# Kernel optimization log

Hardware: AMD Instinct MI355X
Metric: run time of the kernel (lower is better)

The kernel has to match this reference:

```python
import jax, jax.numpy as jnp
import numpy as np

N_NODES = 50000
N_EDGES = 800000
IN_DIM = 512
HID_DIM = 128


def setup_inputs() -> dict:
    key = jax.random.key(0)
    k1, k2, k3 = jax.random.split(key, 3)
    x = jax.random.normal(k1, (N_NODES, IN_DIM), dtype=jnp.float32)
    edge_index = jax.random.randint(k2, (2, N_EDGES), 0, N_NODES, dtype=jnp.int32)
    # GCNConv weight (glorot-ish scale) and bias
    W = jax.random.normal(k3, (IN_DIM, HID_DIM), dtype=jnp.float32) * (1.0 / np.sqrt(IN_DIM))
    b = jnp.zeros((HID_DIM,), dtype=jnp.float32)
    # PReLU per-channel slope, torch default init 0.25
    prelu_w = jnp.full((HID_DIM,), 0.25, dtype=jnp.float32)
    return {"x": x, "edge_index": edge_index, "W": W, "b": b, "prelu_w": prelu_w}


def reference(x, edge_index, W, b, prelu_w):
    N = x.shape[0]
    # 1) linear transform first (GCNConv transforms then aggregates)
    h = x @ W  # [N, H]
    # 2) add self-loops
    loop = jnp.arange(N, dtype=edge_index.dtype)
    src = jnp.concatenate([edge_index[0], loop])  # [E+N]
    dst = jnp.concatenate([edge_index[1], loop])  # [E+N]
    # 3) symmetric degree normalization deg^-1/2 (self-loops guarantee deg>=1)
    deg = jax.ops.segment_sum(jnp.ones_like(dst, dtype=h.dtype), dst, num_segments=N)
    dinv = jax.lax.rsqrt(deg)
    norm = dinv[src] * dinv[dst]  # [E+N]
    # 4) gather-scale-scatter aggregation
    msg = h[src] * norm[:, None]  # [E+N, H]
    out = jax.ops.segment_sum(msg, dst, num_segments=N) + b  # [N, H]
    # 5) per-channel PReLU
    return jnp.where(out > 0, out, prelu_w * out)
```

## Files before the change

kernel.cpp:

```cpp
#include <hip/hip_runtime.h>

#define IN_DIM 512
#define HID 128
#define BK 64

#define RANGE 98
#define NB_ 511
#define NBLK 200
#define SEGCAP 2048

typedef float f4 __attribute__((ext_vector_type(4)));
typedef short bf8 __attribute__((ext_vector_type(8)));

__device__ inline unsigned short f2bf(float f) {
    unsigned u = __float_as_uint(f);
    unsigned r = (u + 0x7FFFu + ((u >> 16) & 1u)) >> 16;
    return (unsigned short)r;
}
__device__ inline float bf2f(unsigned short u) {
    return __uint_as_float(((unsigned)u) << 16);
}
__device__ inline int xcd_perm(int blk) {
    return (blk & 7) * (NBLK / 8) + (blk >> 3);
}

__global__ __launch_bounds__(256) void k_count(const int* __restrict__ dst,
                                               int* __restrict__ cmat, int E) {
    __shared__ int bins[NB_];
    const int blk = blockIdx.x, t = threadIdx.x;
    const int chunk = (((E + NBLK - 1) / NBLK) + 3) & ~3;
    const int start = blk * chunk;
    const int end = min(E, start + chunk);
    for (int i = t; i < NB_; i += 256) bins[i] = 0;
    __syncthreads();
    if (start < E) {
        int nvec = (end - start) >> 2;
        for (int i = t; i < nvec; i += 256) {
            int4 d4 = *(const int4*)(dst + start + i * 4);
            atomicAdd(&bins[d4.x / RANGE], 1);
            atomicAdd(&bins[d4.y / RANGE], 1);
            atomicAdd(&bins[d4.z / RANGE], 1);
            atomicAdd(&bins[d4.w / RANGE], 1);
        }
        for (int i = start + nvec * 4 + t; i < end; i += 256)
            atomicAdd(&bins[dst[i] / RANGE], 1);
    }
    __syncthreads();
    const int p = xcd_perm(blk);
    for (int j = t; j < NB_; j += 256) cmat[j * NBLK + p] = bins[j];
}

__global__ __launch_bounds__(256) void k_cscan(int* __restrict__ cmat,
                                               int* __restrict__ tot) {
    __shared__ int s[256];
    const int j = blockIdx.x, t = threadIdx.x;
    int v = (t < NBLK) ? cmat[j * NBLK + t] : 0;
    s[t] = v;
    __syncthreads();
    for (int off = 1; off < 256; off <<= 1) {
        int y = (t >= off) ? s[t - off] : 0;
        __syncthreads();
        s[t] += y;
        __syncthreads();
    }
    if (t < NBLK) cmat[j * NBLK + t] = s[t] - v;
    if (t == 255) tot[j] = s[255];
}

__global__ __launch_bounds__(512) void k_tscan(const int* __restrict__ tot,
                                               int* __restrict__ bbase,
                                               int* __restrict__ rowStart,
                                               int N, int E) {
    __shared__ int s[512];
    int t = threadIdx.x;
    int v = (t < NB_) ? tot[t] : 0;
    s[t] = v;
    __syncthreads();
    for (int off = 1; off < 512; off <<= 1) {
        int y = (t >= off) ? s[t - off] : 0;
        __syncthreads();
        s[t] += y;
        __syncthreads();
    }
    if (t < NB_) bbase[t] = s[t] - v;
    if (t == 0) rowStart[N] = E;
}

__global__ __launch_bounds__(256) void k_scatter(const int* __restrict__ src,
                                                 const int* __restrict__ dst,
                                                 const int* __restrict__ cmat,
                                                 const int* __restrict__ bbase,
                                                 unsigned* __restrict__ ebuf, int E) {
    __shared__ int cur[NB_];
    const int blk = blockIdx.x, t = threadIdx.x;
    const int p = xcd_perm(blk);
    for (int j = t; j < NB_; j += 256) cur[j] = bbase[j] + cmat[j * NBLK + p];
    __syncthreads();
    const int chunk = (((E + NBLK - 1) / NBLK) + 3) & ~3;
    const int start = blk * chunk;
    const int end = min(E, start + chunk);
    if (start >= E) return;
    int nvec = (end - start) >> 2;
    for (int i = t; i < nvec; i += 256) {
        int4 s4 = *(const int4*)(src + start + i * 4);
        int4 d4 = *(const int4*)(dst + start + i * 4);
        int ss[4] = {s4.x, s4.y, s4.z, s4.w};
        int dd[4] = {d4.x, d4.y, d4.z, d4.w};
#pragma unroll
        for (int k = 0; k < 4; k++) {
            int b = dd[k] / RANGE;
            int ld = dd[k] - b * RANGE;
            int pos = atomicAdd(&cur[b], 1);
            ebuf[pos] = ((unsigned)ld << 25) | (unsigned)ss[k];
        }
    }
    for (int i = start + nvec * 4 + t; i < end; i += 256) {
        int d = dst[i];
        int b = d / RANGE;
        int ld = d - b * RANGE;
        int pos = atomicAdd(&cur[b], 1);
        ebuf[pos] = ((unsigned)ld << 25) | (unsigned)src[i];
    }
}

__global__ __launch_bounds__(256) void k_binfill(const unsigned* __restrict__ ebuf,
                                                 const int* __restrict__ tot,
                                                 const int* __restrict__ bbase,
                                                 int* __restrict__ rowStart,
                                                 float* __restrict__ dinv,
                                                 int* __restrict__ esrc, int N) {
    __shared__ int bins[RANGE];
    __shared__ int cur[RANGE];
    __shared__ int ss[128];
    __shared__ int seg[SEGCAP];
    const int b = blockIdx.x;
    const int t = threadIdx.x;
    const int base = bbase[b];
    const int cnt = min(tot[b], SEGCAP);
    const int n0 = b * RANGE;
    const unsigned* ep = ebuf + base;

    for (int i = t; i < RANGE; i += 256) bins[i] = 0;
    __syncthreads();
    for (int i = t; i < cnt; i += 256) atomicAdd(&bins[ep[i] >> 25], 1);
    __syncthreads();
    int v = (t < RANGE) ? bins[t] : 0;
    if (t < 128) ss[t] = v;
    __syncthreads();
    for (int off = 1; off < 128; off <<= 1) {
        int y = (t >= off && t < 128) ? ss[t - off] : 0;
        __syncthreads();
        if (t < 128) ss[t] += y;
        __syncthreads();
    }
    if (t < RANGE) {
        int ex = ss[t] - v;
        cur[t] = ex;
        int g = n0 + t;
        if (g < N) {
            rowStart[g] = base + ex;
            dinv[g] = rsqrtf((float)(v + 1));
        }
    }
    __syncthreads();
    for (int i = t; i < cnt; i += 256) {
        unsigned w = ep[i];
        int r = atomicAdd(&cur[w >> 25], 1);
        if (r < SEGCAP) seg[r] = (int)(w & 0x1FFFFFFu);
    }
    __syncthreads();
    for (int i = t; i < cnt; i += 256) esrc[base + i] = seg[i];
}

__global__ __launch_bounds__(256) void k_convW(const float* __restrict__ W,
                                               unsigned short* __restrict__ Wt) {
    int id = blockIdx.x * 256 + threadIdx.x;
    int n = id & (HID - 1);
    int k = id >> 7;
    Wt[(size_t)n * IN_DIM + k] = f2bf(W[(size_t)k * HID + n]);
}

__global__ __launch_bounds__(256, 2) void k_gemm(const float* __restrict__ x,
                                                 const unsigned short* __restrict__ Wt,
                                                 unsigned short* __restrict__ h, int M) {
    __shared__ unsigned short As[128][BK + 8];
    __shared__ unsigned short Bs[128][BK + 8];
    const int t = threadIdx.x;
    const int wave = t >> 6, lane = t & 63;
    const int row0 = blockIdx.x * 128;
    const int quad = lane >> 4, l16 = lane & 15;

    f4 acc[2][8];
#pragma unroll
    for (int i = 0; i < 2; i++)
#pragma unroll
        for (int j = 0; j < 8; j++) acc[i][j] = (f4){0.f, 0.f, 0.f, 0.f};

    const int srow = t >> 1;
    const int shalf = t & 1;
    const bool rowok = (row0 + srow) < M;
    const float* xrow = x + (size_t)(row0 + srow) * IN_DIM + shalf * 32;
    const unsigned short* wrow = Wt + (size_t)srow * IN_DIM + shalf * 32;

    for (int k0 = 0; k0 < IN_DIM; k0 += BK) {
        float4 v[8];
#pragma unroll
        for (int i = 0; i < 8; i++)
            v[i] = rowok ? *(const float4*)(xrow + k0 + i * 4)
                         : make_float4(0.f, 0.f, 0.f, 0.f);
        unsigned short tmp[32];
#pragma unroll
        for (int i = 0; i < 8; i++) {
            tmp[i * 4 + 0] = f2bf(v[i].x);
            tmp[i * 4 + 1] = f2bf(v[i].y);
            tmp[i * 4 + 2] = f2bf(v[i].z);
            tmp[i * 4 + 3] = f2bf(v[i].w);
        }
#pragma unroll
        for (int i = 0; i < 4; i++)
            *(float4*)&As[srow][shalf * 32 + i * 8] = *(float4*)&tmp[i * 8];
#pragma unroll
        for (int i = 0; i < 4; i++)
            *(float4*)&Bs[srow][shalf * 32 + i * 8] =
                *(const float4*)(wrow + k0 + i * 8);
        __syncthreads();

#pragma unroll
        for (int ks = 0; ks < BK; ks += 32) {
            bf8 af[2];
#pragma unroll
            for (int rt = 0; rt < 2; rt++)
                af[rt] = *(const bf8*)&As[wave * 32 + rt * 16 + l16][ks + quad * 8];
#pragma unroll
            for (int nt = 0; nt < 8; nt++) {
                bf8 bfv = *(const bf8*)&Bs[nt * 16 + l16][ks + quad * 8];
#pragma unroll
                for (int rt = 0; rt < 2; rt++)
                    acc[rt][nt] = __builtin_amdgcn_mfma_f32_16x16x32_bf16(
                        af[rt], bfv, acc[rt][nt], 0, 0, 0);
            }
        }
        __syncthreads();
    }

#pragma unroll
    for (int rt = 0; rt < 2; rt++) {
#pragma unroll
        for (int reg = 0; reg < 4; reg++) {
            int row = row0 + wave * 32 + rt * 16 + quad * 4 + reg;
            if (row < M) {
#pragma unroll
                for (int nt = 0; nt < 8; nt++) {
                    int col = nt * 16 + l16;
                    h[(size_t)row * HID + col] = f2bf(acc[rt][nt][reg]);
                }
            }
        }
    }
}

__global__ __launch_bounds__(256) void k_pull(const unsigned short* __restrict__ h,
                                              const int* __restrict__ esrc,
                                              const int* __restrict__ rowStart,
                                              const float* __restrict__ dinv,
                                              const float* __restrict__ bias,
                                              const float* __restrict__ pw,
                                              float* __restrict__ out, int N) {
    int gid = blockIdx.x * 256 + threadIdx.x;
    int node = gid >> 5;
    int l = threadIdx.x & 31;
    if (node >= N) return;
    int e0 = rowStart[node], e1 = rowStart[node + 1];
    float di = dinv[node];
    const int ci = l * 4;
    ushort4 hv = *(const ushort4*)&h[(size_t)node * HID + ci];
    float s2 = di * di;
    float ax = bf2f(hv.x) * s2, ay = bf2f(hv.y) * s2;
    float az = bf2f(hv.z) * s2, aw = bf2f(hv.w) * s2;
    int j = e0;
    for (; j + 4 <= e1; j += 4) {
        int s0 = esrc[j], s1 = esrc[j + 1], s2i = esrc[j + 2], s3 = esrc[j + 3];
        float w0 = dinv[s0] * di, w1 = dinv[s1] * di;
        float w2 = dinv[s2i] * di, w3 = dinv[s3] * di;
        ushort4 a0 = *(const ushort4*)&h[(size_t)s0 * HID + ci];
        ushort4 a1 = *(const ushort4*)&h[(size_t)s1 * HID + ci];
        ushort4 a2 = *(const ushort4*)&h[(size_t)s2i * HID + ci];
        ushort4 a3 = *(const ushort4*)&h[(size_t)s3 * HID + ci];
        ax += bf2f(a0.x) * w0 + bf2f(a1.x) * w1 + bf2f(a2.x) * w2 + bf2f(a3.x) * w3;
        ay += bf2f(a0.y) * w0 + bf2f(a1.y) * w1 + bf2f(a2.y) * w2 + bf2f(a3.y) * w3;
        az += bf2f(a0.z) * w0 + bf2f(a1.z) * w1 + bf2f(a2.z) * w2 + bf2f(a3.z) * w3;
        aw += bf2f(a0.w) * w0 + bf2f(a1.w) * w1 + bf2f(a2.w) * w2 + bf2f(a3.w) * w3;
    }
    for (; j < e1; j++) {
        int s = esrc[j];
        float w = dinv[s] * di;
        ushort4 a = *(const ushort4*)&h[(size_t)s * HID + ci];
        ax += bf2f(a.x) * w; ay += bf2f(a.y) * w;
        az += bf2f(a.z) * w; aw += bf2f(a.w) * w;
    }
    float4 bv = *(const float4*)&bias[ci];
    float4 pv = *(const float4*)&pw[ci];
    float ox = ax + bv.x, oy = ay + bv.y, oz = az + bv.z, ow = aw + bv.w;
    ox = ox > 0.f ? ox : pv.x * ox;
    oy = oy > 0.f ? oy : pv.y * oy;
    oz = oz > 0.f ? oz : pv.z * oz;
    ow = ow > 0.f ? ow : pv.w * ow;
    *(float4*)&out[(size_t)node * HID + ci] = make_float4(ox, oy, oz, ow);
}

extern "C" void kernel_launch(void* const* d_in, const int* in_sizes, int n_in,
                              void* d_out, int out_size, void* d_ws, size_t ws_size,
                              hipStream_t stream) {
    const float* x  = (const float*)d_in[0];
    const int*   ei = (const int*)d_in[1];
    const float* W  = (const float*)d_in[2];
    const float* b  = (const float*)d_in[3];
    const float* pw = (const float*)d_in[4];

    const int N = in_sizes[0] / IN_DIM;
    const int E = in_sizes[1] / 2;
    const int* src = ei;
    const int* dst = ei + E;

    char* ws = (char*)d_ws;
    size_t off = 0;
    auto carve = [&](size_t bytes) -> void* {
        void* p = ws + off;
        off = (off + bytes + 255) & ~(size_t)255;
        return p;
    };
    unsigned short* h = (unsigned short*)carve((size_t)N * HID * sizeof(unsigned short));
    int*   rowStart = (int*)carve((size_t)(N + 1) * sizeof(int));
    float* dinv     = (float*)carve((size_t)N * sizeof(float));
    int*   esrc     = (int*)carve((size_t)E * sizeof(int));
    unsigned short* Wt = (unsigned short*)carve((size_t)IN_DIM * HID * sizeof(unsigned short));
    int*   cmat     = (int*)carve((size_t)NB_ * NBLK * sizeof(int));
    int*   tot      = (int*)carve((size_t)NB_ * sizeof(int));
    int*   bbase    = (int*)carve((size_t)NB_ * sizeof(int));
    unsigned* ebuf  = (unsigned*)carve((size_t)E * sizeof(unsigned));

    k_convW<<<(IN_DIM * HID) / 256, 256, 0, stream>>>(W, Wt);
    k_gemm<<<(N + 127) / 128, 256, 0, stream>>>(x, Wt, h, N);
    k_count<<<NBLK, 256, 0, stream>>>(dst, cmat, E);
    k_cscan<<<NB_, 256, 0, stream>>>(cmat, tot);
    k_tscan<<<1, 512, 0, stream>>>(tot, bbase, rowStart, N, E);
    k_scatter<<<NBLK, 256, 0, stream>>>(src, dst, cmat, bbase, ebuf, E);
    k_binfill<<<NB_, 256, 0, stream>>>(ebuf, tot, bbase, rowStart, dinv, esrc, N);
    k_pull<<<(int)(((size_t)N * 32 + 255) / 256), 256, 0, stream>>>(
        h, esrc, rowStart, dinv, b, pw, (float*)d_out, N);
}
```

Measured before the change: 239.1 us.

## Double-buffer GEMM LDS tiles and widen pull gather to 16-byte loads

```diff
diff --git a/kernel.cpp b/kernel.cpp
--- a/kernel.cpp
+++ b/kernel.cpp
@@ -17,9 +17,8 @@
     unsigned r = (u + 0x7FFFu + ((u >> 16) & 1u)) >> 16;
     return (unsigned short)r;
 }
-__device__ inline float bf2f(unsigned short u) {
-    return __uint_as_float(((unsigned)u) << 16);
-}
+__device__ inline float bf_lo(unsigned u) { return __uint_as_float(u << 16); }
+__device__ inline float bf_hi(unsigned u) { return __uint_as_float(u & 0xFFFF0000u); }
 __device__ inline int xcd_perm(int blk) {
     return (blk & 7) * (NBLK / 8) + (blk >> 3);
 }
@@ -183,8 +182,8 @@
 __global__ __launch_bounds__(256, 2) void k_gemm(const float* __restrict__ x,
                                                  const unsigned short* __restrict__ Wt,
                                                  unsigned short* __restrict__ h, int M) {
-    __shared__ unsigned short As[128][BK + 8];
-    __shared__ unsigned short Bs[128][BK + 8];
+    __shared__ unsigned short As[2][128][BK + 8];
+    __shared__ unsigned short Bs[2][128][BK + 8];
     const int t = threadIdx.x;
     const int wave = t >> 6, lane = t & 63;
     const int row0 = blockIdx.x * 128;
@@ -202,12 +201,14 @@
     const float* xrow = x + (size_t)(row0 + srow) * IN_DIM + shalf * 32;
     const unsigned short* wrow = Wt + (size_t)srow * IN_DIM + shalf * 32;
 
-    for (int k0 = 0; k0 < IN_DIM; k0 += BK) {
-        float4 v[8];
-#pragma unroll
-        for (int i = 0; i < 8; i++)
-            v[i] = rowok ? *(const float4*)(xrow + k0 + i * 4)
-                         : make_float4(0.f, 0.f, 0.f, 0.f);
+    float4 v[8], wv[4];
+#pragma unroll
+    for (int i = 0; i < 8; i++)
+        v[i] = rowok ? *(const float4*)(xrow + i * 4) : make_float4(0.f, 0.f, 0.f, 0.f);
+#pragma unroll
+    for (int i = 0; i < 4; i++) wv[i] = *(const float4*)(wrow + i * 8);
+
+    auto stage = [&](int buf) {
         unsigned short tmp[32];
 #pragma unroll
         for (int i = 0; i < 8; i++) {
@@ -218,29 +219,46 @@
         }
 #pragma unroll
         for (int i = 0; i < 4; i++)
-            *(float4*)&As[srow][shalf * 32 + i * 8] = *(float4*)&tmp[i * 8];
+            *(float4*)&As[buf][srow][shalf * 32 + i * 8] = *(float4*)&tmp[i * 8];
 #pragma unroll
         for (int i = 0; i < 4; i++)
-            *(float4*)&Bs[srow][shalf * 32 + i * 8] =
-                *(const float4*)(wrow + k0 + i * 8);
-        __syncthreads();
-
+            *(float4*)&Bs[buf][srow][shalf * 32 + i * 8] = wv[i];
+    };
+
+    stage(0);
+    __syncthreads();
+
+    const int NITER = IN_DIM / BK;
+    for (int it = 0; it < NITER; it++) {
+        const int cur = it & 1;
+        if (it + 1 < NITER) {
+            const int k0 = (it + 1) * BK;
+#pragma unroll
+            for (int i = 0; i < 8; i++)
+                v[i] = rowok ? *(const float4*)(xrow + k0 + i * 4)
+                             : make_float4(0.f, 0.f, 0.f, 0.f);
+#pragma unroll
+            for (int i = 0; i < 4; i++) wv[i] = *(const float4*)(wrow + k0 + i * 8);
+        }
 #pragma unroll
         for (int ks = 0; ks < BK; ks += 32) {
             bf8 af[2];
 #pragma unroll
             for (int rt = 0; rt < 2; rt++)
-                af[rt] = *(const bf8*)&As[wave * 32 + rt * 16 + l16][ks + quad * 8];
+                af[rt] = *(const bf8*)&As[cur][wave * 32 + rt * 16 + l16][ks + quad * 8];
 #pragma unroll
             for (int nt = 0; nt < 8; nt++) {
-                bf8 bfv = *(const bf8*)&Bs[nt * 16 + l16][ks + quad * 8];
+                bf8 bfv = *(const bf8*)&Bs[cur][nt * 16 + l16][ks + quad * 8];
 #pragma unroll
                 for (int rt = 0; rt < 2; rt++)
                     acc[rt][nt] = __builtin_amdgcn_mfma_f32_16x16x32_bf16(
                         af[rt], bfv, acc[rt][nt], 0, 0, 0);
             }
         }
-        __syncthreads();
+        if (it + 1 < NITER) {
+            stage(cur ^ 1);
+            __syncthreads();
+        }
     }
 
 #pragma unroll
@@ -267,45 +285,63 @@
                                               const float* __restrict__ pw,
                                               float* __restrict__ out, int N) {
     int gid = blockIdx.x * 256 + threadIdx.x;
-    int node = gid >> 5;
-    int l = threadIdx.x & 31;
+    int node = gid >> 4;
+    int l = threadIdx.x & 15;
     if (node >= N) return;
     int e0 = rowStart[node], e1 = rowStart[node + 1];
     float di = dinv[node];
-    const int ci = l * 4;
-    ushort4 hv = *(const ushort4*)&h[(size_t)node * HID + ci];
+    const int ci = l * 8;
+    const unsigned short* hrow = h + (size_t)node * HID + ci;
+    uint4 hu = *(const uint4*)hrow;
     float s2 = di * di;
-    float ax = bf2f(hv.x) * s2, ay = bf2f(hv.y) * s2;
-    float az = bf2f(hv.z) * s2, aw = bf2f(hv.w) * s2;
+    float a0 = bf_lo(hu.x) * s2, a1 = bf_hi(hu.x) * s2;
+    float a2 = bf_lo(hu.y) * s2, a3 = bf_hi(hu.y) * s2;
+    float a4 = bf_lo(hu.z) * s2, a5 = bf_hi(hu.z) * s2;
+    float a6 = bf_lo(hu.w) * s2, a7 = bf_hi(hu.w) * s2;
     int j = e0;
     for (; j + 4 <= e1; j += 4) {
         int s0 = esrc[j], s1 = esrc[j + 1], s2i = esrc[j + 2], s3 = esrc[j + 3];
         float w0 = dinv[s0] * di, w1 = dinv[s1] * di;
         float w2 = dinv[s2i] * di, w3 = dinv[s3] * di;
-        ushort4 a0 = *(const ushort4*)&h[(size_t)s0 * HID + ci];
-        ushort4 a1 = *(const ushort4*)&h[(size_t)s1 * HID + ci];
-        ushort4 a2 = *(const ushort4*)&h[(size_t)s2i * HID + ci];
-        ushort4 a3 = *(const ushort4*)&h[(size_t)s3 * HID + ci];
-        ax += bf2f(a0.x) * w0 + bf2f(a1.x) * w1 + bf2f(a2.x) * w2 + bf2f(a3.x) * w3;
-        ay += bf2f(a0.y) * w0 + bf2f(a1.y) * w1 + bf2f(a2.y) * w2 + bf2f(a3.y) * w3;
-        az += bf2f(a0.z) * w0 + bf2f(a1.z) * w1 + bf2f(a2.z) * w2 + bf2f(a3.z) * w3;
-        aw += bf2f(a0.w) * w0 + bf2f(a1.w) * w1 + bf2f(a2.w) * w2 + bf2f(a3.w) * w3;
+        uint4 u0 = *(const uint4*)(h + (size_t)s0 * HID + ci);
+        uint4 u1 = *(const uint4*)(h + (size_t)s1 * HID + ci);
+        uint4 u2 = *(const uint4*)(h + (size_t)s2i * HID + ci);
+        uint4 u3 = *(const uint4*)(h + (size_t)s3 * HID + ci);
+        a0 += bf_lo(u0.x) * w0 + bf_lo(u1.x) * w1 + bf_lo(u2.x) * w2 + bf_lo(u3.x) * w3;
+        a1 += bf_hi(u0.x) * w0 + bf_hi(u1.x) * w1 + bf_hi(u2.x) * w2 + bf_hi(u3.x) * w3;
+        a2 += bf_lo(u0.y) * w0 + bf_lo(u1.y) * w1 + bf_lo(u2.y) * w2 + bf_lo(u3.y) * w3;
+        a3 += bf_hi(u0.y) * w0 + bf_hi(u1.y) * w1 + bf_hi(u2.y) * w2 + bf_hi(u3.y) * w3;
+        a4 += bf_lo(u0.z) * w0 + bf_lo(u1.z) * w1 + bf_lo(u2.z) * w2 + bf_lo(u3.z) * w3;
+        a5 += bf_hi(u0.z) * w0 + bf_hi(u1.z) * w1 + bf_hi(u2.z) * w2 + bf_hi(u3.z) * w3;
+        a6 += bf_lo(u0.w) * w0 + bf_lo(u1.w) * w1 + bf_lo(u2.w) * w2 + bf_lo(u3.w) * w3;
+        a7 += bf_hi(u0.w) * w0 + bf_hi(u1.w) * w1 + bf_hi(u2.w) * w2 + bf_hi(u3.w) * w3;
     }
     for (; j < e1; j++) {
         int s = esrc[j];
         float w = dinv[s] * di;
-        ushort4 a = *(const ushort4*)&h[(size_t)s * HID + ci];
-        ax += bf2f(a.x) * w; ay += bf2f(a.y) * w;
-        az += bf2f(a.z) * w; aw += bf2f(a.w) * w;
-    }
-    float4 bv = *(const float4*)&bias[ci];
-    float4 pv = *(const float4*)&pw[ci];
-    float ox = ax + bv.x, oy = ay + bv.y, oz = az + bv.z, ow = aw + bv.w;
-    ox = ox > 0.f ? ox : pv.x * ox;
-    oy = oy > 0.f ? oy : pv.y * oy;
-    oz = oz > 0.f ? oz : pv.z * oz;
-    ow = ow > 0.f ? ow : pv.w * ow;
-    *(float4*)&out[(size_t)node * HID + ci] = make_float4(ox, oy, oz, ow);
+        uint4 u = *(const uint4*)(h + (size_t)s * HID + ci);
+        a0 += bf_lo(u.x) * w; a1 += bf_hi(u.x) * w;
+        a2 += bf_lo(u.y) * w; a3 += bf_hi(u.y) * w;
+        a4 += bf_lo(u.z) * w; a5 += bf_hi(u.z) * w;
+        a6 += bf_lo(u.w) * w; a7 += bf_hi(u.w) * w;
+    }
+    float4 bv0 = *(const float4*)&bias[ci];
+    float4 bv1 = *(const float4*)&bias[ci + 4];
+    float4 pv0 = *(const float4*)&pw[ci];
+    float4 pv1 = *(const float4*)&pw[ci + 4];
+    float o0 = a0 + bv0.x, o1 = a1 + bv0.y, o2 = a2 + bv0.z, o3 = a3 + bv0.w;
+    float o4 = a4 + bv1.x, o5 = a5 + bv1.y, o6 = a6 + bv1.z, o7 = a7 + bv1.w;
+    o0 = o0 > 0.f ? o0 : pv0.x * o0;
+    o1 = o1 > 0.f ? o1 : pv0.y * o1;
+    o2 = o2 > 0.f ? o2 : pv0.z * o2;
+    o3 = o3 > 0.f ? o3 : pv0.w * o3;
+    o4 = o4 > 0.f ? o4 : pv1.x * o4;
+    o5 = o5 > 0.f ? o5 : pv1.y * o5;
+    o6 = o6 > 0.f ? o6 : pv1.z * o6;
+    o7 = o7 > 0.f ? o7 : pv1.w * o7;
+    float* orow = out + (size_t)node * HID + ci;
+    *(float4*)orow = make_float4(o0, o1, o2, o3);
+    *(float4*)(orow + 4) = make_float4(o4, o5, o6, o7);
 }
 
 extern "C" void kernel_launch(void* const* d_in, const int* in_sizes, int n_in,
@@ -346,6 +382,6 @@
     k_tscan<<<1, 512, 0, stream>>>(tot, bbase, rowStart, N, E);
     k_scatter<<<NBLK, 256, 0, stream>>>(src, dst, cmat, bbase, ebuf, E);
     k_binfill<<<NB_, 256, 0, stream>>>(ebuf, tot, bbase, rowStart, dinv, esrc, N);
-    k_pull<<<(int)(((size_t)N * 32 + 255) / 256), 256, 0, stream>>>(
+    k_pull<<<(int)(((size_t)N * 16 + 255) / 256), 256, 0, stream>>>(
         h, esrc, rowStart, dinv, b, pw, (float*)d_out, N);
 }
```

After: 243.8 us. Within noise of the previous version (+2.0%).
